# Performance work log

Measured on AMD Instinct MI355X. Metric: run time of the kernel, lower is better.

Reference implementation:

```python
import jax, jax.numpy as jnp
import numpy as np

B, M, N, K = 128, 32, 64, 2048  # batch, queue rows, strokes per step, stroke length (K <= M*N)


def setup_inputs() -> dict:
    key = jax.random.key(0)
    ks = jax.random.split(key, 18)
    f32 = jnp.float32
    rn = lambda k, s, sc=1.0: jax.random.normal(k, s, f32) * sc
    return {
        'qt1': rn(ks[0], (B, M, N, 2)),
        'ht1': rn(ks[1], (B, N, 2)),
        'zt': rn(ks[2], (B, N)),
        'alpha_t': jax.random.uniform(ks[3], (B, N), f32),
        'conv_w': rn(ks[4], (2, 2, M + 1, 1), 0.1),  # OIHW, kernel (M+1, 1)
        'conv_b': rn(ks[5], (2,), 0.1),
        'W_xr': rn(ks[6], (2, 2)), 'W_hr': rn(ks[7], (2, 2)), 'b_r': rn(ks[8], (2,)),
        'W_xu': rn(ks[9], (2, 2)), 'W_hu': rn(ks[10], (2, 2)), 'b_u': rn(ks[11], (2,)),
        'W_xn': rn(ks[12], (2, 2)), 'W_hn': rn(ks[13], (2, 2)), 'b_n': rn(ks[14], (2,)),
        'lin_w': rn(ks[15], (N, 2 * N), 0.05),
        'lin_b': rn(ks[16], (N,), 0.05),
        'W_emb': rn(ks[17], (K, 2), 0.1),  # stereo stroke waveform table (stands in for embedding_layer)
    }


def reference(qt1, ht1, zt, alpha_t, conv_w, conv_b, W_xr, W_hr, b_r, W_xu, W_hu, b_u, W_xn, W_hn, b_n, lin_w, lin_b, W_emb):
    Bx = qt1.shape[0]
    # memory matrix: queue + hidden state -> [B, M+1, N, 2]
    Mt1 = jnp.concatenate([qt1, ht1[:, None]], axis=1)
    # full-height (M+1,1) conv over 2 channels, position-wise over N -> [B, N, 2]
    Ht1 = jnp.einsum('bhnc,och->bno', Mt1, conv_w[..., 0]) + conv_b
    xt = jnp.stack([zt, alpha_t], axis=-1)  # [B, N, 2]
    # tiny GRU-style gating on the 2-channel state
    rt = jax.nn.sigmoid(xt @ W_xr + Ht1 @ W_hr + b_r)
    ut = jax.nn.sigmoid(xt @ W_xu + Ht1 @ W_hu + b_u)
    nt = jnp.tanh(xt @ W_xn + (rt * Ht1) @ W_hn + b_n)
    ht = ut * ht1 + (1.0 - ut) * nt  # [B, N, 2]
    it = ht.reshape(Bx, 2 * N) @ lin_w.T + lin_b  # [B, N] stroke intensities
    # embedding: intensity-scaled stroke waveform per onset -> [B, N, K, 2]
    srt = (it * alpha_t)[:, :, None, None] * W_emb[None, None]
    # shifted scatter-accumulate (overlap-add): f_srt[:, i:i+K] += srt[:, i]
    pos = (jnp.arange(N)[:, None] + jnp.arange(K)[None, :]).reshape(-1)  # [N*K]
    f_srt = jnp.zeros((Bx, N + K - 1, 2), srt.dtype).at[:, pos].add(srt.reshape(Bx, N * K, 2))
    st = qt1[:, 0] + f_srt[:, :N]  # emitted samples [B, N, 2]
    # shift queue up one row and add the remaining overlap tail into the flattened queue
    q_shift = jnp.concatenate([qt1[:, 1:], jnp.zeros_like(qt1[:, :1])], axis=1).reshape(Bx, M * N, 2)
    tail = jnp.pad(f_srt[:, N:], ((0, 0), (0, M * N - (K - 1)), (0, 0)))
    qt = (q_shift + tail).reshape(Bx, M, N, 2)
    return st, qt, ht
```

## Files before the change

kernel.cpp:

```cpp
#include <hip/hip_runtime.h>
#include <math.h>

#define NB 128
#define NM 32
#define NN 64
#define NK 2048
#define NP (NN + NK - 1)
#define HALF0 1056
#define NR 2176

__global__ __launch_bounds__(256) void gen_cell_kernel(
    const float* __restrict__ qt1,
    const float* __restrict__ ht1,
    const float* __restrict__ zt,
    const float* __restrict__ alpha_t,
    const float* __restrict__ conv_w,
    const float* __restrict__ conv_b,
    const float* __restrict__ W_xr, const float* __restrict__ W_hr, const float* __restrict__ b_r,
    const float* __restrict__ W_xu, const float* __restrict__ W_hu, const float* __restrict__ b_u,
    const float* __restrict__ W_xn, const float* __restrict__ W_hn, const float* __restrict__ b_n,
    const float* __restrict__ lin_w, const float* __restrict__ lin_b,
    const float* __restrict__ W_emb,
    float* __restrict__ out)
{
    const int b    = blockIdx.x >> 1;
    const int half = blockIdx.x & 1;
    const int tid  = threadIdx.x;

    __shared__ __align__(16) float2 s_wr[NR];
    __shared__ __align__(16) float s_f[2 * HALF0];
    __shared__ __align__(16) float s_ht[2 * NN];
    __shared__ float s_s[NN];

    {
        const float2* w2g = (const float2*)W_emb;
        float2 z2; z2.x = 0.f; z2.y = 0.f;
        for (int i = tid; i < NR; i += 256) {
            float2 v = (i >= 64 && i < 2112) ? w2g[NP - i] : z2;
            s_wr[i] = v;
        }
    }

    float* st_out = out;
    float* qt_out = out + NB * NN * 2;
    float* ht_out = out + NB * NN * 2 + NB * NM * NN * 2;

    if (tid < NN) {
        const int n = tid;
        const float* q = qt1 + (size_t)b * (NM * NN * 2) + n * 2;
        float h0 = conv_b[0], h1 = conv_b[1];
        #pragma unroll
        for (int h = 0; h < NM; ++h) {
            float m0 = q[h * (NN * 2)];
            float m1 = q[h * (NN * 2) + 1];
            h0 = fmaf(m0, conv_w[h],      fmaf(m1, conv_w[33 + h], h0));
            h1 = fmaf(m0, conv_w[66 + h], fmaf(m1, conv_w[99 + h], h1));
        }
        const float hp0 = ht1[b * (NN * 2) + n * 2];
        const float hp1 = ht1[b * (NN * 2) + n * 2 + 1];
        h0 = fmaf(hp0, conv_w[32],      fmaf(hp1, conv_w[33 + 32], h0));
        h1 = fmaf(hp0, conv_w[66 + 32], fmaf(hp1, conv_w[99 + 32], h1));

        const float x0 = zt[b * NN + n];
        const float x1 = alpha_t[b * NN + n];

        float pr0 = x0*W_xr[0] + x1*W_xr[2] + h0*W_hr[0] + h1*W_hr[2] + b_r[0];
        float pr1 = x0*W_xr[1] + x1*W_xr[3] + h0*W_hr[1] + h1*W_hr[3] + b_r[1];
        float r0 = 1.f / (1.f + expf(-pr0));
        float r1 = 1.f / (1.f + expf(-pr1));

        float pu0 = x0*W_xu[0] + x1*W_xu[2] + h0*W_hu[0] + h1*W_hu[2] + b_u[0];
        float pu1 = x0*W_xu[1] + x1*W_xu[3] + h0*W_hu[1] + h1*W_hu[3] + b_u[1];
        float u0 = 1.f / (1.f + expf(-pu0));
        float u1 = 1.f / (1.f + expf(-pu1));

        float g0 = r0 * h0, g1 = r1 * h1;
        float pn0 = x0*W_xn[0] + x1*W_xn[2] + g0*W_hn[0] + g1*W_hn[2] + b_n[0];
        float pn1 = x0*W_xn[1] + x1*W_xn[3] + g0*W_hn[1] + g1*W_hn[3] + b_n[1];
        float nt0 = tanhf(pn0);
        float nt1 = tanhf(pn1);

        float ho0 = u0 * hp0 + (1.f - u0) * nt0;
        float ho1 = u1 * hp1 + (1.f - u1) * nt1;
        s_ht[n * 2]     = ho0;
        s_ht[n * 2 + 1] = ho1;
        if (half == 0) {
            ht_out[b * (NN * 2) + n * 2]     = ho0;
            ht_out[b * (NN * 2) + n * 2 + 1] = ho1;
        }
    }
    __syncthreads();

    if (tid < NN) {
        const int n = tid;
        float acc = lin_b[n];
        const float4* lw4 = (const float4*)(lin_w + n * (2 * NN));
        const float4* h4  = (const float4*)s_ht;
        #pragma unroll
        for (int j = 0; j < 32; ++j) {
            float4 lw = lw4[j];
            float4 hv = h4[j];
            acc = fmaf(lw.x, hv.x, acc);
            acc = fmaf(lw.y, hv.y, acc);
            acc = fmaf(lw.z, hv.z, acc);
            acc = fmaf(lw.w, hv.w, acc);
        }
        s_s[n] = acc * alpha_t[b * NN + n];
    }
    __syncthreads();

    const int plo = half ? HALF0 : 0;
    {
        const int p0 = plo + tid;
        const float2* R0 = s_wr + (NP - p0);
        const float2* R1 = R0 - 256;
        const float2* R2p = R0 - 512;
        const float2* R3 = R0 - 768;
        float a00 = 0.f, a01 = 0.f, a10 = 0.f, a11 = 0.f;
        float a20 = 0.f, a21 = 0.f, a30 = 0.f, a31 = 0.f;
        #pragma unroll 8
        for (int n = 0; n < NN; ++n) {
            float sv = s_s[n];
            float2 w0 = R0[n];
            float2 w1 = R1[n];
            float2 w2v = R2p[n];
            float2 w3 = R3[n];
            a00 = fmaf(sv, w0.x, a00); a01 = fmaf(sv, w0.y, a01);
            a10 = fmaf(sv, w1.x, a10); a11 = fmaf(sv, w1.y, a11);
            a20 = fmaf(sv, w2v.x, a20); a21 = fmaf(sv, w2v.y, a21);
            a30 = fmaf(sv, w3.x, a30); a31 = fmaf(sv, w3.y, a31);
        }
        s_f[tid * 2]              = a00; s_f[tid * 2 + 1]              = a01;
        s_f[(tid + 256) * 2]      = a10; s_f[(tid + 256) * 2 + 1]      = a11;
        s_f[(tid + 512) * 2]      = a20; s_f[(tid + 512) * 2 + 1]      = a21;
        s_f[(tid + 768) * 2]      = a30; s_f[(tid + 768) * 2 + 1]      = a31;
        if (tid < 32) {
            const int p = plo + 1024 + tid;
            const float2* Rt = s_wr + (NP - p);
            float t0 = 0.f, t1 = 0.f;
            #pragma unroll 8
            for (int n = 0; n < NN; ++n) {
                float sv = s_s[n];
                float2 wv = Rt[n];
                t0 = fmaf(sv, wv.x, t0);
                t1 = fmaf(sv, wv.y, t1);
            }
            s_f[(1024 + tid) * 2]     = t0;
            s_f[(1024 + tid) * 2 + 1] = t1;
        }
    }
    __syncthreads();

    if (half == 0 && tid < 128) {
        st_out[b * 128 + tid] = qt1[(size_t)b * 4096 + tid] + s_f[tid];
    }
    {
        const float* qb = qt1 + (size_t)b * 4096;
        float* ob = qt_out + (size_t)b * 4096;
        const int ilo = half ? 496 : 0;
        const int ihi = half ? 1024 : 496;
        const int fofs = 128 - 2 * plo;
        for (int i = ilo + tid; i < ihi; i += 256) {
            int x = i * 4;
            float4 v;
            if (x <= 3964) {
                const float4 qv = *(const float4*)(qb + 128 + x);
                const float4 fv = *(const float4*)(s_f + fofs + x);
                v.x = qv.x + fv.x; v.y = qv.y + fv.y;
                v.z = qv.z + fv.z; v.w = qv.w + fv.w;
            } else {
                float tmp[4];
                #pragma unroll
                for (int c = 0; c < 4; ++c) {
                    int xx = x + c;
                    float qv = (xx < 3968) ? qb[128 + xx] : 0.f;
                    float fv = (xx < 4094) ? s_f[fofs + xx] : 0.f;
                    tmp[c] = qv + fv;
                }
                v.x = tmp[0]; v.y = tmp[1]; v.z = tmp[2]; v.w = tmp[3];
            }
            *(float4*)(ob + x) = v;
        }
    }
}

extern "C" void kernel_launch(void* const* d_in, const int* in_sizes, int n_in,
                              void* d_out, int out_size, void* d_ws, size_t ws_size,
                              hipStream_t stream) {
    (void)in_sizes; (void)n_in; (void)out_size; (void)d_ws; (void)ws_size;
    gen_cell_kernel<<<dim3(NB * 2), dim3(256), 0, stream>>>(
        (const float*)d_in[0],  (const float*)d_in[1],  (const float*)d_in[2],
        (const float*)d_in[3],  (const float*)d_in[4],  (const float*)d_in[5],
        (const float*)d_in[6],  (const float*)d_in[7],  (const float*)d_in[8],
        (const float*)d_in[9],  (const float*)d_in[10], (const float*)d_in[11],
        (const float*)d_in[12], (const float*)d_in[13], (const float*)d_in[14],
        (const float*)d_in[15], (const float*)d_in[16], (const float*)d_in[17],
        (float*)d_out);
}
```

Before: 100.3 us.

## Split each batch's overlap-add across four blocks instead of two

The grid grows from two to four blocks per batch item. Each block now computes a 528-sample quarter of the overlap-add and stages only the matching 591-entry window of the reversed waveform table in shared memory. The goal is more blocks in flight to fill the GPU's compute units, with less shared-memory fill and fewer accumulators per block. The cost is that every block recomputes the conv, GRU and linear prologue, so that redundant work doubles.

```diff
diff --git a/kernel.cpp b/kernel.cpp
--- a/kernel.cpp
+++ b/kernel.cpp
@@ -6,8 +6,9 @@
 #define NN 64
 #define NK 2048
 #define NP (NN + NK - 1)
-#define HALF0 1056
-#define NR 2176
+#define NQ 4
+#define QSZ 528
+#define WSPAN 592
 
 __global__ __launch_bounds__(256) void gen_cell_kernel(
     const float* __restrict__ qt1,
@@ -23,21 +24,24 @@
     const float* __restrict__ W_emb,
     float* __restrict__ out)
 {
-    const int b    = blockIdx.x >> 1;
-    const int half = blockIdx.x & 1;
-    const int tid  = threadIdx.x;
+    const int b   = blockIdx.x >> 2;
+    const int q   = blockIdx.x & 3;
+    const int tid = threadIdx.x;
+    const int plo = q * QSZ;
 
-    __shared__ __align__(16) float2 s_wr[NR];
-    __shared__ __align__(16) float s_f[2 * HALF0];
+    __shared__ __align__(16) float2 s_wr[WSPAN];
+    __shared__ __align__(16) float s_f[2 * QSZ];
     __shared__ __align__(16) float s_ht[2 * NN];
     __shared__ float s_s[NN];
 
     {
         const float2* w2g = (const float2*)W_emb;
+        const int i_min = 1584 - plo;
         float2 z2; z2.x = 0.f; z2.y = 0.f;
-        for (int i = tid; i < NR; i += 256) {
+        for (int j = tid; j < 591; j += 256) {
+            int i = i_min + j;
             float2 v = (i >= 64 && i < 2112) ? w2g[NP - i] : z2;
-            s_wr[i] = v;
+            s_wr[j] = v;
         }
     }
 
@@ -47,12 +51,12 @@
 
     if (tid < NN) {
         const int n = tid;
-        const float* q = qt1 + (size_t)b * (NM * NN * 2) + n * 2;
+        const float* qp = qt1 + (size_t)b * (NM * NN * 2) + n * 2;
         float h0 = conv_b[0], h1 = conv_b[1];
         #pragma unroll
         for (int h = 0; h < NM; ++h) {
-            float m0 = q[h * (NN * 2)];
-            float m1 = q[h * (NN * 2) + 1];
+            float m0 = qp[h * (NN * 2)];
+            float m1 = qp[h * (NN * 2) + 1];
             h0 = fmaf(m0, conv_w[h],      fmaf(m1, conv_w[33 + h], h0));
             h1 = fmaf(m0, conv_w[66 + h], fmaf(m1, conv_w[99 + h], h1));
         }
@@ -84,7 +88,7 @@
         float ho1 = u1 * hp1 + (1.f - u1) * nt1;
         s_ht[n * 2]     = ho0;
         s_ht[n * 2 + 1] = ho1;
-        if (half == 0) {
+        if (q == 0) {
             ht_out[b * (NN * 2) + n * 2]     = ho0;
             ht_out[b * (NN * 2) + n * 2 + 1] = ho1;
         }
@@ -109,34 +113,22 @@
     }
     __syncthreads();
 
-    const int plo = half ? HALF0 : 0;
     {
-        const int p0 = plo + tid;
-        const float2* R0 = s_wr + (NP - p0);
+        const float2* R0 = s_wr + (527 - tid);
         const float2* R1 = R0 - 256;
-        const float2* R2p = R0 - 512;
-        const float2* R3 = R0 - 768;
         float a00 = 0.f, a01 = 0.f, a10 = 0.f, a11 = 0.f;
-        float a20 = 0.f, a21 = 0.f, a30 = 0.f, a31 = 0.f;
         #pragma unroll 8
         for (int n = 0; n < NN; ++n) {
             float sv = s_s[n];
             float2 w0 = R0[n];
             float2 w1 = R1[n];
-            float2 w2v = R2p[n];
-            float2 w3 = R3[n];
             a00 = fmaf(sv, w0.x, a00); a01 = fmaf(sv, w0.y, a01);
             a10 = fmaf(sv, w1.x, a10); a11 = fmaf(sv, w1.y, a11);
-            a20 = fmaf(sv, w2v.x, a20); a21 = fmaf(sv, w2v.y, a21);
-            a30 = fmaf(sv, w3.x, a30); a31 = fmaf(sv, w3.y, a31);
         }
-        s_f[tid * 2]              = a00; s_f[tid * 2 + 1]              = a01;
-        s_f[(tid + 256) * 2]      = a10; s_f[(tid + 256) * 2 + 1]      = a11;
-        s_f[(tid + 512) * 2]      = a20; s_f[(tid + 512) * 2 + 1]      = a21;
-        s_f[(tid + 768) * 2]      = a30; s_f[(tid + 768) * 2 + 1]      = a31;
-        if (tid < 32) {
-            const int p = plo + 1024 + tid;
-            const float2* Rt = s_wr + (NP - p);
+        s_f[tid * 2]             = a00; s_f[tid * 2 + 1]             = a01;
+        s_f[(tid + 256) * 2]     = a10; s_f[(tid + 256) * 2 + 1]     = a11;
+        if (tid < 16 && (plo + 512 + tid) < NP) {
+            const float2* Rt = s_wr + (527 - 512 - tid);
             float t0 = 0.f, t1 = 0.f;
             #pragma unroll 8
             for (int n = 0; n < NN; ++n) {
@@ -145,20 +137,20 @@
                 t0 = fmaf(sv, wv.x, t0);
                 t1 = fmaf(sv, wv.y, t1);
             }
-            s_f[(1024 + tid) * 2]     = t0;
-            s_f[(1024 + tid) * 2 + 1] = t1;
+            s_f[(512 + tid) * 2]     = t0;
+            s_f[(512 + tid) * 2 + 1] = t1;
         }
     }
     __syncthreads();
 
-    if (half == 0 && tid < 128) {
+    if (q == 0 && tid < 128) {
         st_out[b * 128 + tid] = qt1[(size_t)b * 4096 + tid] + s_f[tid];
     }
     {
         const float* qb = qt1 + (size_t)b * 4096;
         float* ob = qt_out + (size_t)b * 4096;
-        const int ilo = half ? 496 : 0;
-        const int ihi = half ? 1024 : 496;
+        const int ilo = (q == 0) ? 0 : (q * 1056 - 128) / 4;
+        const int ihi = (q == 3) ? 1024 : (q * 1056 + 928) / 4;
         const int fofs = 128 - 2 * plo;
         for (int i = ilo + tid; i < ihi; i += 256) {
             int x = i * 4;
@@ -188,7 +180,7 @@
                               void* d_out, int out_size, void* d_ws, size_t ws_size,
                               hipStream_t stream) {
     (void)in_sizes; (void)n_in; (void)out_size; (void)d_ws; (void)ws_size;
-    gen_cell_kernel<<<dim3(NB * 2), dim3(256), 0, stream>>>(
+    gen_cell_kernel<<<dim3(NB * NQ), dim3(256), 0, stream>>>(
         (const float*)d_in[0],  (const float*)d_in[1],  (const float*)d_in[2],
         (const float*)d_in[3],  (const float*)d_in[4],  (const float*)d_in[5],
         (const float*)d_in[6],  (const float*)d_in[7],  (const float*)d_in[8],
```

Measured after the change: 99.92 us. No clear change (-0.3%).
